# Kernel optimization log

Hardware: AMD Instinct MI355X
Metric: run time of the kernel (lower is better)

Reference implementation:

```python
import jax, jax.numpy as jnp
import numpy as np

B, J, D = 2048, 22, 128

def setup_inputs() -> dict:
    key = jax.random.key(0)
    k1, k2, k3 = jax.random.split(key, 3)
    src = jax.random.normal(k1, (B, J, D), dtype=jnp.float32)
    W = jax.random.normal(k2, (D, D), dtype=jnp.float32) * (1.0 / np.sqrt(D))
    b = jax.random.normal(k3, (D,), dtype=jnp.float32) * 0.01
    return {"src": src, "W": W, "b": b}

def reference(src, W, b):
    # Path-based accumulation sum_k (src[path[k+1]] - src[path[k]]) telescopes
    # to src[:, j, :] - src[:, i, :] for the shortest path i -> j.
    # pairwise[b, i, j, :] = src[b, j, :] - src[b, i, :]
    pairwise = src[:, None, :, :] - src[:, :, None, :]  # [B, J, J, D]
    # nn.Linear on last dim: x @ W^T + b
    return jnp.einsum('bijd,ed->bije', pairwise, W) + b
```

## Files before the change

kernel.cpp:

```cpp
#include <hip/hip_runtime.h>

#define NB 2048
#define NJ 22
#define ND 128
#define ROW4 (NJ * ND / 4)

typedef float f32x4 __attribute__((ext_vector_type(4)));

__global__ __launch_bounds__(256, 4) void see_kernel(
    const float* __restrict__ src, const float* __restrict__ W,
    const float* __restrict__ bias, float* __restrict__ out) {
  __shared__ float srcS[NJ * ND];
  __shared__ float YS[NJ * ND];

  const int b = blockIdx.x;
  const int t = threadIdx.x;
  const float* srcB = src + (size_t)b * NJ * ND;

  for (int idx = t; idx < NJ * ND / 4; idx += 256) {
    reinterpret_cast<f32x4*>(srcS)[idx] =
        reinterpret_cast<const f32x4*>(srcB)[idx];
  }

  const int e  = t & 127;
  const int dh = t >> 7;

  float w[64];
  {
    const f32x4* Wrow = reinterpret_cast<const f32x4*>(W + e * ND + dh * 64);
#pragma unroll
    for (int k = 0; k < 16; ++k) {
      f32x4 v = Wrow[k];
      w[4 * k + 0] = v.x;
      w[4 * k + 1] = v.y;
      w[4 * k + 2] = v.z;
      w[4 * k + 3] = v.w;
    }
  }
  __syncthreads();

  for (int c = 0; c < 2; ++c) {
    float acc[11];
#pragma unroll
    for (int jj = 0; jj < 11; ++jj) {
      const int j = c * 11 + jj;
      const f32x4* s4 = reinterpret_cast<const f32x4*>(srcS + j * ND + dh * 64);
      float a = 0.f;
#pragma unroll
      for (int k = 0; k < 16; ++k) {
        f32x4 s = s4[k];
        a += s.x * w[4 * k + 0];
        a += s.y * w[4 * k + 1];
        a += s.z * w[4 * k + 2];
        a += s.w * w[4 * k + 3];
      }
      acc[jj] = a;
    }
    if (dh == 0) {
#pragma unroll
      for (int jj = 0; jj < 11; ++jj) YS[(c * 11 + jj) * ND + e] = acc[jj];
    }
    __syncthreads();
    if (dh == 1) {
#pragma unroll
      for (int jj = 0; jj < 11; ++jj) YS[(c * 11 + jj) * ND + e] += acc[jj];
    }
  }
  __syncthreads();

  const int e4 = t & 31;
  const int j0 = t >> 5;
  const f32x4* YS4 = reinterpret_cast<const f32x4*>(YS);
  const f32x4 bb4 = reinterpret_cast<const f32x4*>(bias)[e4];

  f32x4 yj0 = YS4[j0 * 32 + e4];
  f32x4 yj1 = YS4[(j0 + 8) * 32 + e4];
  f32x4 yj2 = {0.f, 0.f, 0.f, 0.f};
  if (j0 < 6) yj2 = YS4[(j0 + 16) * 32 + e4];
  yj0 += bb4;
  yj1 += bb4;
  yj2 += bb4;

  f32x4* outB4 = reinterpret_cast<f32x4*>(out + (size_t)b * NJ * NJ * ND);

  for (int ii = 0; ii < NJ; ++ii) {
    f32x4 yi = YS4[ii * 32 + e4];
    f32x4* outRow4 = outB4 + (size_t)ii * ROW4;
    f32x4 r0 = yj0 - yi;
    f32x4 r1 = yj1 - yi;
    __builtin_nontemporal_store(r0, outRow4 + t);
    __builtin_nontemporal_store(r1, outRow4 + t + 256);
    if (j0 < 6) {
      f32x4 r2 = yj2 - yi;
      __builtin_nontemporal_store(r2, outRow4 + t + 512);
    }
  }
}

extern "C" void kernel_launch(void* const* d_in, const int* in_sizes, int n_in,
                              void* d_out, int out_size, void* d_ws, size_t ws_size,
                              hipStream_t stream) {
  const float* src  = (const float*)d_in[0];
  const float* W    = (const float*)d_in[1];
  const float* bias = (const float*)d_in[2];
  float* out = (float*)d_out;

  see_kernel<<<NB, 256, 0, stream>>>(src, W, bias, out);
}
```

Before: 111.4 us.

## Split fused kernel into GEMM and broadcast-expand kernels via workspace

Splits the single kernel into two launches. The first computes Y = src·W^T per batch and writes it to the workspace. The second reloads Y, adds the bias, and writes the pairwise differences using regular stores instead of nontemporal ones, with a higher occupancy hint. The aim is to keep the register-heavy GEMM from limiting occupancy during the store-bound expand phase. The cost is a second launch plus an extra round trip of Y through global memory, and the switch to regular stores may change cache behaviour on the large output.

```diff
diff --git a/kernel.cpp b/kernel.cpp
--- a/kernel.cpp
+++ b/kernel.cpp
@@ -4,12 +4,13 @@
 #define NJ 22
 #define ND 128
 #define ROW4 (NJ * ND / 4)
+#define YB4  (NJ * ND / 4)
 
 typedef float f32x4 __attribute__((ext_vector_type(4)));
 
-__global__ __launch_bounds__(256, 4) void see_kernel(
+__global__ __launch_bounds__(256, 4) void gemm_y(
     const float* __restrict__ src, const float* __restrict__ W,
-    const float* __restrict__ bias, float* __restrict__ out) {
+    float* __restrict__ Y) {
   __shared__ float srcS[NJ * ND];
   __shared__ float YS[NJ * ND];
 
@@ -68,32 +69,46 @@
   }
   __syncthreads();
 
+  f32x4* Yb4 = reinterpret_cast<f32x4*>(Y + (size_t)b * NJ * ND);
+  const f32x4* YS4 = reinterpret_cast<const f32x4*>(YS);
+  Yb4[t] = YS4[t];
+  Yb4[t + 256] = YS4[t + 256];
+  if (t < 192) Yb4[t + 512] = YS4[t + 512];
+}
+
+__global__ __launch_bounds__(256, 8) void expand(
+    const float* __restrict__ Y, const float* __restrict__ bias,
+    float* __restrict__ out) {
+  __shared__ float YS[NJ * ND];
+
+  const int b = blockIdx.x;
+  const int t = threadIdx.x;
+
+  const f32x4* Yb4 = reinterpret_cast<const f32x4*>(Y + (size_t)b * NJ * ND);
+  f32x4* YS4w = reinterpret_cast<f32x4*>(YS);
+  YS4w[t] = Yb4[t];
+  YS4w[t + 256] = Yb4[t + 256];
+  if (t < 192) YS4w[t + 512] = Yb4[t + 512];
+  __syncthreads();
+
   const int e4 = t & 31;
   const int j0 = t >> 5;
   const f32x4* YS4 = reinterpret_cast<const f32x4*>(YS);
   const f32x4 bb4 = reinterpret_cast<const f32x4*>(bias)[e4];
 
-  f32x4 yj0 = YS4[j0 * 32 + e4];
-  f32x4 yj1 = YS4[(j0 + 8) * 32 + e4];
+  f32x4 yj0 = YS4[j0 * 32 + e4] + bb4;
+  f32x4 yj1 = YS4[(j0 + 8) * 32 + e4] + bb4;
   f32x4 yj2 = {0.f, 0.f, 0.f, 0.f};
-  if (j0 < 6) yj2 = YS4[(j0 + 16) * 32 + e4];
-  yj0 += bb4;
-  yj1 += bb4;
-  yj2 += bb4;
+  if (j0 < 6) yj2 = YS4[(j0 + 16) * 32 + e4] + bb4;
 
   f32x4* outB4 = reinterpret_cast<f32x4*>(out + (size_t)b * NJ * NJ * ND);
 
   for (int ii = 0; ii < NJ; ++ii) {
     f32x4 yi = YS4[ii * 32 + e4];
     f32x4* outRow4 = outB4 + (size_t)ii * ROW4;
-    f32x4 r0 = yj0 - yi;
-    f32x4 r1 = yj1 - yi;
-    __builtin_nontemporal_store(r0, outRow4 + t);
-    __builtin_nontemporal_store(r1, outRow4 + t + 256);
-    if (j0 < 6) {
-      f32x4 r2 = yj2 - yi;
-      __builtin_nontemporal_store(r2, outRow4 + t + 512);
-    }
+    outRow4[t] = yj0 - yi;
+    outRow4[t + 256] = yj1 - yi;
+    if (j0 < 6) outRow4[t + 512] = yj2 - yi;
   }
 }
 
@@ -104,6 +119,8 @@
   const float* W    = (const float*)d_in[1];
   const float* bias = (const float*)d_in[2];
   float* out = (float*)d_out;
+  float* Yw  = (float*)d_ws;
 
-  see_kernel<<<NB, 256, 0, stream>>>(src, W, bias, out);
+  gemm_y<<<NB, 256, 0, stream>>>(src, W, Yw);
+  expand<<<NB, 256, 0, stream>>>(Yw, bias, out);
 }
```

Measured after the change: 135.8 us. +21.9%, slower.

## Read src directly via uniform scalar loads and use regular stores

Applied to the files above, without the earlier changes.

Drops the shared-memory staging of src and the sync that follows it. src is now read straight from global memory, with the half index made wave-uniform through readfirstlane so the compiler can use scalar loads. Output stores switch from nontemporal to ordinary stores, and the bias add is folded into the loads. This removes LDS traffic and one barrier, but relies on scalar-load codegen and changes how the large output write interacts with the cache.

```diff
diff --git a/kernel.cpp b/kernel.cpp
--- a/kernel.cpp
+++ b/kernel.cpp
@@ -10,20 +10,12 @@
 __global__ __launch_bounds__(256, 4) void see_kernel(
     const float* __restrict__ src, const float* __restrict__ W,
     const float* __restrict__ bias, float* __restrict__ out) {
-  __shared__ float srcS[NJ * ND];
   __shared__ float YS[NJ * ND];
 
   const int b = blockIdx.x;
   const int t = threadIdx.x;
-  const float* srcB = src + (size_t)b * NJ * ND;
-
-  for (int idx = t; idx < NJ * ND / 4; idx += 256) {
-    reinterpret_cast<f32x4*>(srcS)[idx] =
-        reinterpret_cast<const f32x4*>(srcB)[idx];
-  }
-
-  const int e  = t & 127;
-  const int dh = t >> 7;
+  const int e = t & 127;
+  const int dh = __builtin_amdgcn_readfirstlane(t >> 7);
 
   float w[64];
   {
@@ -37,23 +29,17 @@
       w[4 * k + 3] = v.w;
     }
   }
-  __syncthreads();
+
+  const float* srcU = src + (size_t)b * NJ * ND + dh * 64;
 
   for (int c = 0; c < 2; ++c) {
     float acc[11];
 #pragma unroll
     for (int jj = 0; jj < 11; ++jj) {
-      const int j = c * 11 + jj;
-      const f32x4* s4 = reinterpret_cast<const f32x4*>(srcS + j * ND + dh * 64);
+      const float* sr = srcU + (c * 11 + jj) * ND;
       float a = 0.f;
 #pragma unroll
-      for (int k = 0; k < 16; ++k) {
-        f32x4 s = s4[k];
-        a += s.x * w[4 * k + 0];
-        a += s.y * w[4 * k + 1];
-        a += s.z * w[4 * k + 2];
-        a += s.w * w[4 * k + 3];
-      }
+      for (int k = 0; k < 64; ++k) a += sr[k] * w[k];
       acc[jj] = a;
     }
     if (dh == 0) {
@@ -73,27 +59,19 @@
   const f32x4* YS4 = reinterpret_cast<const f32x4*>(YS);
   const f32x4 bb4 = reinterpret_cast<const f32x4*>(bias)[e4];
 
-  f32x4 yj0 = YS4[j0 * 32 + e4];
-  f32x4 yj1 = YS4[(j0 + 8) * 32 + e4];
+  f32x4 yj0 = YS4[j0 * 32 + e4] + bb4;
+  f32x4 yj1 = YS4[(j0 + 8) * 32 + e4] + bb4;
   f32x4 yj2 = {0.f, 0.f, 0.f, 0.f};
-  if (j0 < 6) yj2 = YS4[(j0 + 16) * 32 + e4];
-  yj0 += bb4;
-  yj1 += bb4;
-  yj2 += bb4;
+  if (j0 < 6) yj2 = YS4[(j0 + 16) * 32 + e4] + bb4;
 
   f32x4* outB4 = reinterpret_cast<f32x4*>(out + (size_t)b * NJ * NJ * ND);
 
   for (int ii = 0; ii < NJ; ++ii) {
     f32x4 yi = YS4[ii * 32 + e4];
     f32x4* outRow4 = outB4 + (size_t)ii * ROW4;
-    f32x4 r0 = yj0 - yi;
-    f32x4 r1 = yj1 - yi;
-    __builtin_nontemporal_store(r0, outRow4 + t);
-    __builtin_nontemporal_store(r1, outRow4 + t + 256);
-    if (j0 < 6) {
-      f32x4 r2 = yj2 - yi;
-      __builtin_nontemporal_store(r2, outRow4 + t + 512);
-    }
+    outRow4[t] = yj0 - yi;
+    outRow4[t + 256] = yj1 - yi;
+    if (j0 < 6) outRow4[t + 512] = yj2 - yi;
   }
 }
 
```

Result: slower. 173.1 us (+55.4%).
